# Kernel tuning notes

Measured on AMD Instinct MI355X. Metric: run time of the kernel, lower is better.

Reference implementation:

```python
import jax, jax.numpy as jnp
import numpy as np


def setup_inputs() -> dict:
    key = jax.random.key(0)
    k1, k2 = jax.random.split(key)
    decoder_state_t = jax.random.normal(k1, (32, 256), dtype=jnp.float32)
    encoder_states = jax.random.normal(k2, (32, 8192, 256), dtype=jnp.float32)
    return {"decoder_state_t": decoder_state_t, "encoder_states": encoder_states}


def reference(decoder_state_t, encoder_states):
    # score[b, s] = sum_h decoder_state_t[b, h] * encoder_states[b, s, h]
    score = jnp.einsum("bh,bsh->bs", decoder_state_t, encoder_states)
    atten_prob = jax.nn.softmax(score, axis=-1)            # (bs, source_length)
    # context[b, h] = sum_s atten_prob[b, s] * encoder_states[b, s, h]
    context = jnp.einsum("bs,bsh->bh", atten_prob, encoder_states)
    return (atten_prob, context)
```

## Files before the change

### kernel.cpp

```cpp
#include <hip/hip_runtime.h>
#include <math.h>

#define B_ 32
#define S_ 8192
#define H_ 256
#define CHUNK_ 256
#define WAVES_PB 4
#define WROWS (CHUNK_ / WAVES_PB)
#define TILE_ 16
#define NCHUNK (S_ / CHUNK_)
#define NBLK (B_ * NCHUNK)
#define PPB NCHUNK

#define CREF 40.0f

__global__ __launch_bounds__(256) void
k1_flash(const float* __restrict__ dec, const float* __restrict__ enc,
         float* __restrict__ scores_out, float* __restrict__ pl,
         float* __restrict__ pc) {
    const int lane  = threadIdx.x & 63;
    const int wave  = threadIdx.x >> 6;
    const int batch = blockIdx.x >> 5;
    const int chunk = blockIdx.x & (NCHUNK - 1);
    const int rowBase = chunk * CHUNK_ + wave * WROWS;

    const float4 d = *(const float4*)(dec + batch * H_ + lane * 4);
    const float* ebase = enc + (size_t)batch * S_ * H_;

    float  l = 0.f;
    float4 c = make_float4(0.f, 0.f, 0.f, 0.f);

    for (int t = 0; t < WROWS / TILE_; ++t) {
        const int r0 = rowBase + t * TILE_;
        float4 v[TILE_];
        float  sc[TILE_];
#pragma unroll
        for (int r = 0; r < TILE_; ++r) {
            v[r] = *(const float4*)(ebase + (size_t)(r0 + r) * H_ + lane * 4);
            float sp = v[r].x * d.x + v[r].y * d.y + v[r].z * d.z + v[r].w * d.w;
#pragma unroll
            for (int off = 32; off; off >>= 1) sp += __shfl_xor(sp, off);
            sc[r] = sp;
            const float p = __expf(sp - CREF);
            l += p;
            c.x += p * v[r].x;
            c.y += p * v[r].y;
            c.z += p * v[r].z;
            c.w += p * v[r].w;
        }
        if (lane == 0) {
            float* so = scores_out + batch * S_ + r0;
            *(float4*)(so + 0)  = make_float4(sc[0],  sc[1],  sc[2],  sc[3]);
            *(float4*)(so + 4)  = make_float4(sc[4],  sc[5],  sc[6],  sc[7]);
            *(float4*)(so + 8)  = make_float4(sc[8],  sc[9],  sc[10], sc[11]);
            *(float4*)(so + 12) = make_float4(sc[12], sc[13], sc[14], sc[15]);
        }
    }

    __shared__ float  sm_l[WAVES_PB];
    __shared__ float4 smc[WAVES_PB][64];
    smc[wave][lane] = c;
    if (lane == 0) sm_l[wave] = l;
    __syncthreads();
    if (wave == 0) {
        float4 s = smc[0][lane];
#pragma unroll
        for (int i = 1; i < WAVES_PB; ++i) {
            s.x += smc[i][lane].x; s.y += smc[i][lane].y;
            s.z += smc[i][lane].z; s.w += smc[i][lane].w;
        }
        *(float4*)(pc + (size_t)blockIdx.x * H_ + lane * 4) = s;
    }
    if (threadIdx.x == 0)
        pl[blockIdx.x] = sm_l[0] + sm_l[1] + sm_l[2] + sm_l[3];
}

__global__ __launch_bounds__(256) void
k23_finish(const float* __restrict__ pl, const float* __restrict__ pc,
           float* __restrict__ probs, float* __restrict__ ctx_out) {
    const int lane = threadIdx.x & 63;
    const int b = (blockIdx.x < 256) ? (blockIdx.x >> 3) : (blockIdx.x - 256);

    float L = (lane < PPB) ? pl[b * PPB + lane] : 0.f;
#pragma unroll
    for (int off = 32; off; off >>= 1) L += __shfl_xor(L, off);
    const float R = 1.f / L;

    if (blockIdx.x < 256) {
        float* p = probs + b * S_ + (blockIdx.x & 7) * 1024 + threadIdx.x * 4;
        float4 v = *(const float4*)p;
        v.x = __expf(v.x - CREF) * R;
        v.y = __expf(v.y - CREF) * R;
        v.z = __expf(v.z - CREF) * R;
        v.w = __expf(v.w - CREF) * R;
        *(float4*)p = v;
    } else {
        const int h = threadIdx.x;
        float acc = 0.f;
        const float* pcb = pc + (size_t)b * PPB * H_ + h;
#pragma unroll 8
        for (int i = 0; i < PPB; ++i)
            acc += pcb[(size_t)i * H_];
        ctx_out[b * H_ + h] = acc * R;
    }
}

extern "C" void kernel_launch(void* const* d_in, const int* in_sizes, int n_in,
                              void* d_out, int out_size, void* d_ws, size_t ws_size,
                              hipStream_t stream) {
    const float* dec = (const float*)d_in[0];
    const float* enc = (const float*)d_in[1];
    float* out   = (float*)d_out;
    float* probs = out;
    float* ctx   = out + B_ * S_;

    float* pl = (float*)d_ws;
    float* pc = pl + NBLK;

    k1_flash<<<NBLK, 256, 0, stream>>>(dec, enc, probs, pl, pc);
    k23_finish<<<256 + B_, 256, 0, stream>>>(pl, pc, probs, ctx);
}
```

Measured before the change: 50.09 us.

## Split each wave into four 16-lane row groups to shorten score reductions

Each wave now processes four rows at a time, one per 16-lane group, with each lane holding 16 hidden elements across four float4 registers. The dot-product reduction needs only four shuffle steps instead of six. Each row is still fully accumulated into per-lane context registers, and a cross-group shuffle reduction at the end folds the four groups together. This raises register use (16 float4 loaded per tile plus 4 context accumulators) and replaces vectorized score stores with scattered scalar stores.

New measurement: 54.22 us. +8.2%, slower.

```diff
diff --git a/kernel.cpp b/kernel.cpp
--- a/kernel.cpp
+++ b/kernel.cpp
@@ -7,7 +7,6 @@
 #define CHUNK_ 256
 #define WAVES_PB 4
 #define WROWS (CHUNK_ / WAVES_PB)
-#define TILE_ 16
 #define NCHUNK (S_ / CHUNK_)
 #define NBLK (B_ * NCHUNK)
 #define PPB NCHUNK
@@ -20,59 +19,95 @@
          float* __restrict__ pc) {
     const int lane  = threadIdx.x & 63;
     const int wave  = threadIdx.x >> 6;
+    const int g     = lane >> 4;
+    const int i     = lane & 15;
     const int batch = blockIdx.x >> 5;
     const int chunk = blockIdx.x & (NCHUNK - 1);
     const int rowBase = chunk * CHUNK_ + wave * WROWS;
 
-    const float4 d = *(const float4*)(dec + batch * H_ + lane * 4);
+    float4 dd[4];
+#pragma unroll
+    for (int k = 0; k < 4; ++k)
+        dd[k] = *(const float4*)(dec + batch * H_ + k * 64 + i * 4);
+
     const float* ebase = enc + (size_t)batch * S_ * H_;
 
     float  l = 0.f;
-    float4 c = make_float4(0.f, 0.f, 0.f, 0.f);
+    float4 c[4];
+#pragma unroll
+    for (int k = 0; k < 4; ++k) c[k] = make_float4(0.f, 0.f, 0.f, 0.f);
 
-    for (int t = 0; t < WROWS / TILE_; ++t) {
-        const int r0 = rowBase + t * TILE_;
-        float4 v[TILE_];
-        float  sc[TILE_];
+    for (int t = 0; t < WROWS / 16; ++t) {
+        const int rT = rowBase + t * 16;
+        float4 v[4][4];
 #pragma unroll
-        for (int r = 0; r < TILE_; ++r) {
-            v[r] = *(const float4*)(ebase + (size_t)(r0 + r) * H_ + lane * 4);
-            float sp = v[r].x * d.x + v[r].y * d.y + v[r].z * d.z + v[r].w * d.w;
+        for (int rg = 0; rg < 4; ++rg)
 #pragma unroll
-            for (int off = 32; off; off >>= 1) sp += __shfl_xor(sp, off);
-            sc[r] = sp;
+            for (int k = 0; k < 4; ++k)
+                v[rg][k] = *(const float4*)(ebase +
+                    (size_t)(rT + rg * 4 + g) * H_ + k * 64 + i * 4);
+
+#pragma unroll
+        for (int rg = 0; rg < 4; ++rg) {
+            float sp = v[rg][0].x * dd[0].x;
+            sp = fmaf(v[rg][0].y, dd[0].y, sp);
+            sp = fmaf(v[rg][0].z, dd[0].z, sp);
+            sp = fmaf(v[rg][0].w, dd[0].w, sp);
+#pragma unroll
+            for (int k = 1; k < 4; ++k) {
+                sp = fmaf(v[rg][k].x, dd[k].x, sp);
+                sp = fmaf(v[rg][k].y, dd[k].y, sp);
+                sp = fmaf(v[rg][k].z, dd[k].z, sp);
+                sp = fmaf(v[rg][k].w, dd[k].w, sp);
+            }
+            sp += __shfl_xor(sp, 1);
+            sp += __shfl_xor(sp, 2);
+            sp += __shfl_xor(sp, 4);
+            sp += __shfl_xor(sp, 8);
+            if (i == 0)
+                scores_out[batch * S_ + rT + rg * 4 + g] = sp;
             const float p = __expf(sp - CREF);
             l += p;
-            c.x += p * v[r].x;
-            c.y += p * v[r].y;
-            c.z += p * v[r].z;
-            c.w += p * v[r].w;
-        }
-        if (lane == 0) {
-            float* so = scores_out + batch * S_ + r0;
-            *(float4*)(so + 0)  = make_float4(sc[0],  sc[1],  sc[2],  sc[3]);
-            *(float4*)(so + 4)  = make_float4(sc[4],  sc[5],  sc[6],  sc[7]);
-            *(float4*)(so + 8)  = make_float4(sc[8],  sc[9],  sc[10], sc[11]);
-            *(float4*)(so + 12) = make_float4(sc[12], sc[13], sc[14], sc[15]);
+#pragma unroll
+            for (int k = 0; k < 4; ++k) {
+                c[k].x += p * v[rg][k].x;
+                c[k].y += p * v[rg][k].y;
+                c[k].z += p * v[rg][k].z;
+                c[k].w += p * v[rg][k].w;
+            }
         }
     }
 
+#pragma unroll
+    for (int k = 0; k < 4; ++k) {
+        c[k].x += __shfl_xor(c[k].x, 16); c[k].x += __shfl_xor(c[k].x, 32);
+        c[k].y += __shfl_xor(c[k].y, 16); c[k].y += __shfl_xor(c[k].y, 32);
+        c[k].z += __shfl_xor(c[k].z, 16); c[k].z += __shfl_xor(c[k].z, 32);
+        c[k].w += __shfl_xor(c[k].w, 16); c[k].w += __shfl_xor(c[k].w, 32);
+    }
+    l += __shfl_xor(l, 16);
+    l += __shfl_xor(l, 32);
+
+    __shared__ float4 smc[WAVES_PB][16][4];
     __shared__ float  sm_l[WAVES_PB];
-    __shared__ float4 smc[WAVES_PB][64];
-    smc[wave][lane] = c;
+    if (g == 0) {
+#pragma unroll
+        for (int k = 0; k < 4; ++k) smc[wave][i][k] = c[k];
+    }
     if (lane == 0) sm_l[wave] = l;
     __syncthreads();
     if (wave == 0) {
-        float4 s = smc[0][lane];
+        const int kk = lane >> 4, ii = lane & 15;
+        float4 s = smc[0][ii][kk];
 #pragma unroll
-        for (int i = 1; i < WAVES_PB; ++i) {
-            s.x += smc[i][lane].x; s.y += smc[i][lane].y;
-            s.z += smc[i][lane].z; s.w += smc[i][lane].w;
+        for (int w = 1; w < WAVES_PB; ++w) {
+            s.x += smc[w][ii][kk].x; s.y += smc[w][ii][kk].y;
+            s.z += smc[w][ii][kk].z; s.w += smc[w][ii][kk].w;
         }
-        *(float4*)(pc + (size_t)blockIdx.x * H_ + lane * 4) = s;
+        *(float4*)(pc + (size_t)blockIdx.x * H_ + kk * 64 + ii * 4) = s;
+        if (lane == 0)
+            pl[blockIdx.x] = sm_l[0] + sm_l[1] + sm_l[2] + sm_l[3];
     }
-    if (threadIdx.x == 0)
-        pl[blockIdx.x] = sm_l[0] + sm_l[1] + sm_l[2] + sm_l[3];
 }
 
 __global__ __launch_bounds__(256) void
```
